# Performance work log

Hardware: AMD Instinct MI355X
Metric: run time of the kernel (lower is better)

The kernel has to match this reference:

```python
import jax, jax.numpy as jnp
import numpy as np

DIM = 768
NUM_HEADS = 12
HEAD_DIM = DIM // NUM_HEADS
ALL_HEAD_DIM = HEAD_DIM * NUM_HEADS
SCALE = HEAD_DIM ** -0.5


def setup_inputs() -> dict:
    key = jax.random.key(0)
    k1, k2, k3, k4 = jax.random.split(key, 4)
    B, N = 8, 1024
    x = jax.random.normal(k1, (B, N, DIM), dtype=jnp.float32)
    # qkv_bias=False -> no qkv bias; proj has bias (nn.Linear default)
    w_qkv = jax.random.normal(k2, (DIM, 3 * ALL_HEAD_DIM), dtype=jnp.float32) * (DIM ** -0.5)
    w_proj = jax.random.normal(k3, (ALL_HEAD_DIM, DIM), dtype=jnp.float32) * (ALL_HEAD_DIM ** -0.5)
    b_proj = jax.random.normal(k4, (DIM,), dtype=jnp.float32) * 0.02
    return {"x": x, "w_qkv": w_qkv, "w_proj": w_proj, "b_proj": b_proj}


def reference(x, w_qkv, w_proj, b_proj):
    B, N, C = x.shape
    qkv = (x @ w_qkv).reshape(B, N, 3, NUM_HEADS, HEAD_DIM)
    qkv = jnp.transpose(qkv, (2, 0, 3, 1, 4))  # [3, B, H, N, D]
    q, k, v = qkv[0], qkv[1], qkv[2]
    attn = jax.nn.softmax(jnp.einsum('bhnd,bhmd->bhnm', q * SCALE, k), axis=-1)
    out = jnp.einsum('bhnm,bhmd->bhnd', attn, v)  # [B, H, N, D]
    out = jnp.transpose(out, (0, 2, 1, 3)).reshape(B, N, ALL_HEAD_DIM)
    return out @ w_proj + b_proj
```

## Files before the change

kernel.cpp:

```cpp
#include <hip/hip_runtime.h>
#include <hip/hip_bf16.h>

#define NH 12
#define HD 64
#define SEQ 1024
#define BATCH 8
#define DIM 768
#define QKVN 2304
#define ROWS 8192

typedef __bf16 bf16x8 __attribute__((ext_vector_type(8)));
typedef float f32x4 __attribute__((ext_vector_type(4)));
typedef unsigned short u16x8 __attribute__((ext_vector_type(8)));
typedef unsigned short u16x4 __attribute__((ext_vector_type(4)));
typedef short s16x4 __attribute__((ext_vector_type(4)));

__device__ __forceinline__ unsigned short f2bf(float f) {
  union { float f; unsigned int u; } c; c.f = f;
  unsigned int u = c.u;
  u += 0x7fffu + ((u >> 16) & 1u);
  return (unsigned short)(u >> 16);
}

__device__ __forceinline__ unsigned int pk_bf16(float a, float b) {
  union { __hip_bfloat162 h; unsigned int w; } u;
  u.h = __float22bfloat162_rn(float2{a, b});
  return u.w;
}

__device__ __forceinline__ float exp2_fast(float x) {
  float r;
  asm("v_exp_f32 %0, %1" : "=v"(r) : "v"(x));
  return r;
}

__device__ __forceinline__ void gload_lds16(const unsigned short* g, unsigned short* l) {
  __builtin_amdgcn_global_load_lds(
      (const __attribute__((address_space(1))) void*)g,
      (__attribute__((address_space(3))) void*)l, 16, 0, 0);
}

__device__ __forceinline__ void tr_tile(const float* __restrict__ src, unsigned short* __restrict__ dst,
                                        int R, int C, int bx, int by, float tile[32][33]) {
  int tx = threadIdx.x & 31, ty = threadIdx.x >> 5;
  int c0 = bx * 32, r0 = by * 32;
#pragma unroll
  for (int i = 0; i < 4; ++i)
    tile[ty + i * 8][tx] = src[(size_t)(r0 + ty + i * 8) * C + c0 + tx];
  __syncthreads();
#pragma unroll
  for (int i = 0; i < 4; ++i)
    dst[(size_t)(c0 + ty + i * 8) * R + r0 + tx] = f2bf(tile[tx][ty + i * 8]);
}

__global__ void prep_kernel(const float* __restrict__ x, unsigned short* __restrict__ xb,
                            const float* __restrict__ w_qkv, unsigned short* __restrict__ wqkvT,
                            const float* __restrict__ w_proj, unsigned short* __restrict__ wprojT) {
  __shared__ float tile[32][33];
  int blk = blockIdx.x;
  if (blk < 6144) {
    int i = blk * 256 + threadIdx.x;
    float4 v = ((const float4*)x)[i];
    unsigned int lo = pk_bf16(v.x, v.y), hi = pk_bf16(v.z, v.w);
    union { unsigned int w[2]; u16x4 o; } u; u.w[0] = lo; u.w[1] = hi;
    ((u16x4*)xb)[i] = u.o;
  } else if (blk < 6144 + 1728) {
    int t = blk - 6144;
    tr_tile(w_qkv, wqkvT, DIM, QKVN, t % 72, t / 72, tile);
  } else {
    int t = blk - 6144 - 1728;
    tr_tile(w_proj, wprojT, DIM, DIM, t % 24, t / 24, tile);
  }
}

template <bool BF16_OUT, bool SCALE_Q>
__global__ __launch_bounds__(256, 3) void gemm192(
    const unsigned short* __restrict__ A, const unsigned short* __restrict__ BT,
    void* __restrict__ Cout, const float* __restrict__ bias,
    int M, int N, int K, int nbyXCD) {
  __shared__ unsigned short As[2][128 * 32];
  __shared__ unsigned short Bs[2][192 * 32];
  const int tid = threadIdx.x;
  const int wave = tid >> 6, lane = tid & 63, quad = lane >> 4, l16 = lane & 15;
  const int wm = wave >> 1, wn = wave & 1;
  const int g = blockIdx.x & 7, bi = blockIdx.x >> 3;
  const int by = g * nbyXCD + (bi % nbyXCD);
  const int bx = bi / nbyXCD;
  const int bm = by * 128, bn = bx * 192;

  const int r0 = tid >> 2, kc0 = (tid & 3) * 8;
  const unsigned short* Ag = A + (size_t)(bm + r0) * K + kc0;
  const unsigned short* Bg = BT + (size_t)(bn + r0) * K + kc0;
  unsigned short* AsB = &As[0][0];
  unsigned short* BsB = &Bs[0][0];
  const int wdst = (tid & ~63) * 8;

#define STAGE_G(kt, b) do {                                                   \
    int koff_ = (kt) * 32;                                                    \
    gload_lds16(Ag + koff_,                    AsB + (b) * 4096 + wdst);      \
    gload_lds16(Ag + koff_ + (size_t)64 * K,   AsB + (b) * 4096 + wdst + 2048);\
    gload_lds16(Bg + koff_,                    BsB + (b) * 6144 + wdst);      \
    gload_lds16(Bg + koff_ + (size_t)64 * K,   BsB + (b) * 6144 + wdst + 2048);\
    gload_lds16(Bg + koff_ + (size_t)128 * K,  BsB + (b) * 6144 + wdst + 4096);\
  } while (0)

  f32x4 zero4 = {0.f, 0.f, 0.f, 0.f};
  f32x4 acc[4][6];
#pragma unroll
  for (int i = 0; i < 4; ++i)
#pragma unroll
    for (int j = 0; j < 6; ++j) acc[i][j] = zero4;

  const int nkt = K >> 5;
  STAGE_G(0, 0);
  for (int kt = 0; kt < nkt; ++kt) {
    __syncthreads();
    if (kt + 1 < nkt) STAGE_G(kt + 1, (kt + 1) & 1);
    const unsigned short* Ab = AsB + (kt & 1) * 4096;
    const unsigned short* Bb = BsB + (kt & 1) * 6144;
    bf16x8 af[4], bf[6];
#pragma unroll
    for (int mt = 0; mt < 4; ++mt)
      af[mt] = *(const bf16x8*)&Ab[(wm * 64 + mt * 16 + l16) * 32 + quad * 8];
#pragma unroll
    for (int nt = 0; nt < 6; ++nt)
      bf[nt] = *(const bf16x8*)&Bb[(wn * 96 + nt * 16 + l16) * 32 + quad * 8];
#pragma unroll
    for (int mt = 0; mt < 4; ++mt)
#pragma unroll
      for (int nt = 0; nt < 6; ++nt)
        acc[mt][nt] = __builtin_amdgcn_mfma_f32_16x16x32_bf16(af[mt], bf[nt], acc[mt][nt], 0, 0, 0);
  }
#undef STAGE_G

#pragma unroll
  for (int mt = 0; mt < 4; ++mt)
#pragma unroll
    for (int nt = 0; nt < 6; ++nt) {
      int col = bn + wn * 96 + nt * 16 + l16;
      float bv = BF16_OUT ? 0.f : bias[col];
      float scl = (SCALE_Q && col < DIM) ? 0.18033688011112042f : 1.0f;
#pragma unroll
      for (int r = 0; r < 4; ++r) {
        int row = bm + wm * 64 + mt * 16 + quad * 4 + r;
        float v = acc[mt][nt][r];
        if (BF16_OUT)
          ((unsigned short*)Cout)[(size_t)row * N + col] = f2bf(v * scl);
        else
          ((float*)Cout)[(size_t)row * N + col] = v + bv;
      }
    }
}

__global__ __launch_bounds__(256, 4) void gemm64_proj(
    const unsigned short* __restrict__ A, const unsigned short* __restrict__ BT,
    float* __restrict__ Cout, const float* __restrict__ bias,
    int M, int N, int K, int nbyXCD) {
  __shared__ unsigned short As[2][128 * 64];
  __shared__ unsigned short Bs[2][64 * 64];
  const int tid = threadIdx.x;
  const int wave = tid >> 6, lane = tid & 63, quad = lane >> 4, l16 = lane & 15;
  const int g = blockIdx.x & 7, bi = blockIdx.x >> 3;
  const int by = g * nbyXCD + (bi % nbyXCD);
  const int bx = bi / nbyXCD;
  const int bm = by * 128, bn = bx * 64;

  const int r0 = tid >> 3;
  const int csw = ((tid & 7) ^ (r0 & 7)) * 8;
  const unsigned short* Ag = A + (size_t)(bm + r0) * K + csw;
  const unsigned short* Bg = BT + (size_t)(bn + r0) * K + csw;
  unsigned short* AsB = &As[0][0];
  unsigned short* BsB = &Bs[0][0];
  const int wdst = (tid & ~63) * 8;

#define STAGE_P(kt, b) do {                                                     \
    int koff_ = (kt) * 64;                                                      \
    gload_lds16(Ag + koff_,                   AsB + (b) * 8192 + wdst);         \
    gload_lds16(Ag + koff_ + (size_t)32 * K,  AsB + (b) * 8192 + wdst + 2048);  \
    gload_lds16(Ag + koff_ + (size_t)64 * K,  AsB + (b) * 8192 + wdst + 4096);  \
    gload_lds16(Ag + koff_ + (size_t)96 * K,  AsB + (b) * 8192 + wdst + 6144);  \
    gload_lds16(Bg + koff_,                   BsB + (b) * 4096 + wdst);         \
    gload_lds16(Bg + koff_ + (size_t)32 * K,  BsB + (b) * 4096 + wdst + 2048);  \
  } while (0)

  f32x4 zero4 = {0.f, 0.f, 0.f, 0.f};
  f32x4 acc[2][4];
#pragma unroll
  for (int i = 0; i < 2; ++i)
#pragma unroll
    for (int j = 0; j < 4; ++j) acc[i][j] = zero4;

  const int nkt = K >> 6;
  STAGE_P(0, 0);
  for (int kt = 0; kt < nkt; ++kt) {
    __syncthreads();
    if (kt + 1 < nkt) STAGE_P(kt + 1, (kt + 1) & 1);
    const unsigned short* Ab = AsB + (kt & 1) * 8192;
    const unsigned short* Bb = BsB + (kt & 1) * 4096;
#pragma unroll
    for (int kk = 0; kk < 2; ++kk) {
      const int pc = ((kk * 4 + quad) ^ (l16 & 7)) * 8;
      bf16x8 af[2], bf[4];
#pragma unroll
      for (int mt = 0; mt < 2; ++mt)
        af[mt] = *(const bf16x8*)&Ab[(wave * 32 + mt * 16 + l16) * 64 + pc];
#pragma unroll
      for (int nt = 0; nt < 4; ++nt)
        bf[nt] = *(const bf16x8*)&Bb[(nt * 16 + l16) * 64 + pc];
#pragma unroll
      for (int mt = 0; mt < 2; ++mt)
#pragma unroll
        for (int nt = 0; nt < 4; ++nt)
          acc[mt][nt] = __builtin_amdgcn_mfma_f32_16x16x32_bf16(af[mt], bf[nt], acc[mt][nt], 0, 0, 0);
    }
  }
#undef STAGE_P

#pragma unroll
  for (int mt = 0; mt < 2; ++mt)
#pragma unroll
    for (int nt = 0; nt < 4; ++nt) {
      int col = bn + nt * 16 + l16;
      float bv = bias[col];
#pragma unroll
      for (int r = 0; r < 4; ++r) {
        int row = bm + wave * 32 + mt * 16 + quad * 4 + r;
        Cout[(size_t)row * N + col] = acc[mt][nt][r] + bv;
      }
    }
}

#define VS 76
__global__ __launch_bounds__(512, 6) void attn_kernel(
    const unsigned short* __restrict__ qkv, unsigned short* __restrict__ out) {
  __shared__ unsigned short Ks[2][64 * 64];
  __shared__ unsigned short Vts[2][64 * VS];

  const int tid = threadIdx.x;
  const int wave = tid >> 6, lane = tid & 63, quad = lane >> 4, l16 = lane & 15;
  const int x = blockIdx.x;
  const int qt = (x >> 3) & 7;
  const int bh = (x & 7) + 8 * (x >> 6);
  const int b = bh / NH, h = bh % NH;
  const int qcol = h * HD, kcol = DIM + h * HD, vcol = 2 * DIM + h * HD;
  const int rowQ0 = b * SEQ + qt * 128;
  const int rowKV0 = b * SEQ;

  const int kk_s = tid >> 8, rem_s = tid & 255, n_s = rem_s >> 2, kc_s = rem_s & 3;
  const unsigned short* kgp = qkv + (size_t)(rowKV0 + n_s) * QKVN + kcol + kk_s * 32 + kc_s * 8;
  unsigned short* klp = &Ks[0][0] + (tid & ~63) * 8;
  const int vn = tid & 63, vd0 = (tid >> 6) * 8;
  const unsigned short* vgp = qkv + (size_t)(rowKV0 + vn) * QKVN + vcol + vd0;

  bf16x8 qf[2];
  {
    const unsigned short* qp = qkv + (size_t)(rowQ0 + wave * 16 + l16) * QKVN + qcol + quad * 8;
    qf[0] = *(const bf16x8*)qp;
    qf[1] = *(const bf16x8*)(qp + 32);
  }

  gload_lds16(kgp, klp);
  {
    u16x8 v0 = *(const u16x8*)vgp;
    unsigned short* vb = &Vts[0][0];
#pragma unroll
    for (int e = 0; e < 8; ++e)
      vb[(vd0 + e) * VS + vn] = v0[e];
  }

  f32x4 zero4 = {0.f, 0.f, 0.f, 0.f};
  f32x4 o[4];
#pragma unroll
  for (int dt = 0; dt < 4; ++dt) o[dt] = zero4;
  float lsum = 0.f;

  for (int jt = 0; jt < 16; ++jt) {
    __syncthreads();
    u16x8 vnext;
    if (jt < 15) {
      gload_lds16(kgp + (size_t)(jt + 1) * 64 * QKVN, klp + ((jt + 1) & 1) * 4096);
      vnext = *(const u16x8*)(vgp + (size_t)(jt + 1) * 64 * QKVN);
    }

    const unsigned short* Kb = &Ks[jt & 1][0];
    const unsigned short* Vb = &Vts[jt & 1][0];

    f32x4 s[4];
#pragma unroll
    for (int nt = 0; nt < 4; ++nt) s[nt] = zero4;
    __builtin_amdgcn_s_setprio(1);
#pragma unroll
    for (int kk = 0; kk < 2; ++kk)
#pragma unroll
      for (int nt = 0; nt < 4; ++nt) {
        bf16x8 kf = *(const bf16x8*)&Kb[kk * 2048 + (nt * 16 + l16) * 32 + quad * 8];
        s[nt] = __builtin_amdgcn_mfma_f32_16x16x32_bf16(kf, qf[kk], s[nt], 0, 0, 0);
      }
    __builtin_amdgcn_s_setprio(0);

    s16x4 pf[4];
#pragma unroll
    for (int nt = 0; nt < 4; ++nt) {
      float p0 = exp2_fast(s[nt][0]);
      float p1 = exp2_fast(s[nt][1]);
      float p2 = exp2_fast(s[nt][2]);
      float p3 = exp2_fast(s[nt][3]);
      lsum += (p0 + p1) + (p2 + p3);
      union { unsigned int w[2]; s16x4 v; } u;
      u.w[0] = pk_bf16(p0, p1);
      u.w[1] = pk_bf16(p2, p3);
      pf[nt] = u.v;
    }

    __builtin_amdgcn_s_setprio(1);
#pragma unroll
    for (int nt = 0; nt < 4; ++nt)
#pragma unroll
      for (int dt = 0; dt < 4; ++dt) {
        s16x4 vv = *(const s16x4*)&Vb[(dt * 16 + l16) * VS + nt * 16 + quad * 4];
        o[dt] = __builtin_amdgcn_mfma_f32_16x16x16bf16_1k(pf[nt], vv, o[dt], 0, 0, 0);
      }
    __builtin_amdgcn_s_setprio(0);

    if (jt < 15) {
      unsigned short* vb = &Vts[(jt + 1) & 1][0];
#pragma unroll
      for (int e = 0; e < 8; ++e)
        vb[(vd0 + e) * VS + vn] = vnext[e];
    }
  }

  float l = lsum;
  l += __shfl_xor(l, 16);
  l += __shfl_xor(l, 32);
#pragma unroll
  for (int r = 0; r < 4; ++r) {
    float inv = 1.f / __shfl(l, quad * 4 + r);
    int row = rowQ0 + wave * 16 + quad * 4 + r;
#pragma unroll
    for (int dt = 0; dt < 4; ++dt)
      out[(size_t)row * DIM + h * HD + dt * 16 + l16] = f2bf(o[dt][r] * inv);
  }
}

extern "C" void kernel_launch(void* const* d_in, const int* in_sizes, int n_in,
                              void* d_out, int out_size, void* d_ws, size_t ws_size,
                              hipStream_t stream) {
  const float* x = (const float*)d_in[0];
  const float* w_qkv = (const float*)d_in[1];
  const float* w_proj = (const float*)d_in[2];
  const float* b_proj = (const float*)d_in[3];
  float* outp = (float*)d_out;

  unsigned short* xb = (unsigned short*)d_ws;
  unsigned short* wqkvT = xb + (size_t)ROWS * DIM;
  unsigned short* wprojT = wqkvT + (size_t)QKVN * DIM;
  unsigned short* qkvb = wprojT + (size_t)DIM * DIM;
  unsigned short* attnb = xb;

  prep_kernel<<<dim3(6144 + 1728 + 576), 256, 0, stream>>>(x, xb, w_qkv, wqkvT, w_proj, wprojT);
  gemm192<true, true><<<dim3(768), 256, 0, stream>>>(xb, wqkvT, qkvb, nullptr, ROWS, QKVN, DIM, 8);
  attn_kernel<<<dim3(8 * 96), 512, 0, stream>>>(qkvb, attnb);
  gemm64_proj<<<dim3(768), 256, 0, stream>>>(attnb, wprojT, outp, b_proj, ROWS, DIM, DIM, 8);
}
```

Before: 177.7 us.

## Split attention keys across wave pairs so each K/V fragment feeds two query subtiles

Waves are paired. Each pair owns 32 query rows, and each wave in the pair handles half of every 64-key tile. Every K fragment and V fragment read from LDS now feeds two MFMAs, one per 16-row query subtile, which roughly halves LDS read traffic per unit of MFMA work. The two half-results, the partial O accumulators and row sums, are combined at the end through an LDS scratch area that reuses the K/V buffers. The cost is an extra sync and reduction step and twice as many accumulator registers per wave.

```diff
diff --git a/kernel.cpp b/kernel.cpp
--- a/kernel.cpp
+++ b/kernel.cpp
@@ -233,11 +233,13 @@
 #define VS 76
 __global__ __launch_bounds__(512, 6) void attn_kernel(
     const unsigned short* __restrict__ qkv, unsigned short* __restrict__ out) {
-  __shared__ unsigned short Ks[2][64 * 64];
-  __shared__ unsigned short Vts[2][64 * VS];
+  __shared__ unsigned short lds[2 * 64 * 64 + 2 * 64 * VS];
+  unsigned short* Ks = lds;
+  unsigned short* Vts = lds + 2 * 64 * 64;
 
   const int tid = threadIdx.x;
   const int wave = tid >> 6, lane = tid & 63, quad = lane >> 4, l16 = lane & 15;
+  const int qg = wave >> 1, kh = wave & 1;
   const int x = blockIdx.x;
   const int qt = (x >> 3) & 7;
   const int bh = (x & 7) + 8 * (x >> 6);
@@ -248,31 +250,34 @@
 
   const int kk_s = tid >> 8, rem_s = tid & 255, n_s = rem_s >> 2, kc_s = rem_s & 3;
   const unsigned short* kgp = qkv + (size_t)(rowKV0 + n_s) * QKVN + kcol + kk_s * 32 + kc_s * 8;
-  unsigned short* klp = &Ks[0][0] + (tid & ~63) * 8;
+  unsigned short* klp = Ks + (tid & ~63) * 8;
   const int vn = tid & 63, vd0 = (tid >> 6) * 8;
   const unsigned short* vgp = qkv + (size_t)(rowKV0 + vn) * QKVN + vcol + vd0;
 
-  bf16x8 qf[2];
-  {
-    const unsigned short* qp = qkv + (size_t)(rowQ0 + wave * 16 + l16) * QKVN + qcol + quad * 8;
-    qf[0] = *(const bf16x8*)qp;
-    qf[1] = *(const bf16x8*)(qp + 32);
+  bf16x8 qf[2][2];
+#pragma unroll
+  for (int sub = 0; sub < 2; ++sub) {
+    const unsigned short* qp = qkv + (size_t)(rowQ0 + qg * 32 + sub * 16 + l16) * QKVN + qcol + quad * 8;
+    qf[sub][0] = *(const bf16x8*)qp;
+    qf[sub][1] = *(const bf16x8*)(qp + 32);
   }
 
   gload_lds16(kgp, klp);
   {
     u16x8 v0 = *(const u16x8*)vgp;
-    unsigned short* vb = &Vts[0][0];
+    unsigned short* vb = Vts;
 #pragma unroll
     for (int e = 0; e < 8; ++e)
       vb[(vd0 + e) * VS + vn] = v0[e];
   }
 
   f32x4 zero4 = {0.f, 0.f, 0.f, 0.f};
-  f32x4 o[4];
-#pragma unroll
-  for (int dt = 0; dt < 4; ++dt) o[dt] = zero4;
-  float lsum = 0.f;
+  f32x4 o[2][4];
+#pragma unroll
+  for (int sub = 0; sub < 2; ++sub)
+#pragma unroll
+    for (int dt = 0; dt < 4; ++dt) o[sub][dt] = zero4;
+  float lsum[2] = {0.f, 0.f};
 
   for (int jt = 0; jt < 16; ++jt) {
     __syncthreads();
@@ -282,64 +287,98 @@
       vnext = *(const u16x8*)(vgp + (size_t)(jt + 1) * 64 * QKVN);
     }
 
-    const unsigned short* Kb = &Ks[jt & 1][0];
-    const unsigned short* Vb = &Vts[jt & 1][0];
-
-    f32x4 s[4];
-#pragma unroll
-    for (int nt = 0; nt < 4; ++nt) s[nt] = zero4;
+    const unsigned short* Kb = Ks + (jt & 1) * 4096;
+    const unsigned short* Vb = Vts + (jt & 1) * (64 * VS);
+
+    f32x4 s[2][2];
+#pragma unroll
+    for (int sub = 0; sub < 2; ++sub)
+#pragma unroll
+      for (int nt = 0; nt < 2; ++nt) s[sub][nt] = zero4;
     __builtin_amdgcn_s_setprio(1);
 #pragma unroll
     for (int kk = 0; kk < 2; ++kk)
 #pragma unroll
-      for (int nt = 0; nt < 4; ++nt) {
-        bf16x8 kf = *(const bf16x8*)&Kb[kk * 2048 + (nt * 16 + l16) * 32 + quad * 8];
-        s[nt] = __builtin_amdgcn_mfma_f32_16x16x32_bf16(kf, qf[kk], s[nt], 0, 0, 0);
+      for (int nt = 0; nt < 2; ++nt) {
+        bf16x8 kf = *(const bf16x8*)&Kb[kk * 2048 + (kh * 32 + nt * 16 + l16) * 32 + quad * 8];
+        s[0][nt] = __builtin_amdgcn_mfma_f32_16x16x32_bf16(kf, qf[0][kk], s[0][nt], 0, 0, 0);
+        s[1][nt] = __builtin_amdgcn_mfma_f32_16x16x32_bf16(kf, qf[1][kk], s[1][nt], 0, 0, 0);
       }
     __builtin_amdgcn_s_setprio(0);
 
-    s16x4 pf[4];
-#pragma unroll
-    for (int nt = 0; nt < 4; ++nt) {
-      float p0 = exp2_fast(s[nt][0]);
-      float p1 = exp2_fast(s[nt][1]);
-      float p2 = exp2_fast(s[nt][2]);
-      float p3 = exp2_fast(s[nt][3]);
-      lsum += (p0 + p1) + (p2 + p3);
-      union { unsigned int w[2]; s16x4 v; } u;
-      u.w[0] = pk_bf16(p0, p1);
-      u.w[1] = pk_bf16(p2, p3);
-      pf[nt] = u.v;
-    }
+    s16x4 pf[2][2];
+#pragma unroll
+    for (int sub = 0; sub < 2; ++sub)
+#pragma unroll
+      for (int nt = 0; nt < 2; ++nt) {
+        float p0 = exp2_fast(s[sub][nt][0]);
+        float p1 = exp2_fast(s[sub][nt][1]);
+        float p2 = exp2_fast(s[sub][nt][2]);
+        float p3 = exp2_fast(s[sub][nt][3]);
+        lsum[sub] += (p0 + p1) + (p2 + p3);
+        union { unsigned int w[2]; s16x4 v; } u;
+        u.w[0] = pk_bf16(p0, p1);
+        u.w[1] = pk_bf16(p2, p3);
+        pf[sub][nt] = u.v;
+      }
 
     __builtin_amdgcn_s_setprio(1);
 #pragma unroll
-    for (int nt = 0; nt < 4; ++nt)
+    for (int nt = 0; nt < 2; ++nt)
 #pragma unroll
       for (int dt = 0; dt < 4; ++dt) {
-        s16x4 vv = *(const s16x4*)&Vb[(dt * 16 + l16) * VS + nt * 16 + quad * 4];
-        o[dt] = __builtin_amdgcn_mfma_f32_16x16x16bf16_1k(pf[nt], vv, o[dt], 0, 0, 0);
+        s16x4 vv = *(const s16x4*)&Vb[(dt * 16 + l16) * VS + kh * 32 + nt * 16 + quad * 4];
+        o[0][dt] = __builtin_amdgcn_mfma_f32_16x16x16bf16_1k(pf[0][nt], vv, o[0][dt], 0, 0, 0);
+        o[1][dt] = __builtin_amdgcn_mfma_f32_16x16x16bf16_1k(pf[1][nt], vv, o[1][dt], 0, 0, 0);
       }
     __builtin_amdgcn_s_setprio(0);
 
     if (jt < 15) {
-      unsigned short* vb = &Vts[(jt + 1) & 1][0];
+      unsigned short* vb = Vts + ((jt + 1) & 1) * (64 * VS);
 #pragma unroll
       for (int e = 0; e < 8; ++e)
         vb[(vd0 + e) * VS + vn] = vnext[e];
     }
   }
 
-  float l = lsum;
-  l += __shfl_xor(l, 16);
-  l += __shfl_xor(l, 32);
-#pragma unroll
-  for (int r = 0; r < 4; ++r) {
-    float inv = 1.f / __shfl(l, quad * 4 + r);
-    int row = rowQ0 + wave * 16 + quad * 4 + r;
-#pragma unroll
-    for (int dt = 0; dt < 4; ++dt)
-      out[(size_t)row * DIM + h * HD + dt * 16 + l16] = f2bf(o[dt][r] * inv);
+  __syncthreads();
+  float* sc = (float*)lds;
+  float* scl = sc + 4 * 64 * 32;
+  if (kh) {
+    float* dst = sc + (qg * 64 + lane) * 32;
+#pragma unroll
+    for (int sub = 0; sub < 2; ++sub)
+#pragma unroll
+      for (int dt = 0; dt < 4; ++dt)
+        *(f32x4*)(dst + sub * 16 + dt * 4) = o[sub][dt];
+    scl[(qg * 64 + lane) * 2 + 0] = lsum[0];
+    scl[(qg * 64 + lane) * 2 + 1] = lsum[1];
+  }
+  __syncthreads();
+  if (!kh) {
+    const float* src = sc + (qg * 64 + lane) * 32;
+#pragma unroll
+    for (int sub = 0; sub < 2; ++sub)
+#pragma unroll
+      for (int dt = 0; dt < 4; ++dt)
+        o[sub][dt] += *(const f32x4*)(src + sub * 16 + dt * 4);
+    lsum[0] += scl[(qg * 64 + lane) * 2 + 0];
+    lsum[1] += scl[(qg * 64 + lane) * 2 + 1];
+
+#pragma unroll
+    for (int sub = 0; sub < 2; ++sub) {
+      float l = lsum[sub];
+      l += __shfl_xor(l, 16);
+      l += __shfl_xor(l, 32);
+#pragma unroll
+      for (int r = 0; r < 4; ++r) {
+        float inv = 1.f / __shfl(l, quad * 4 + r);
+        int row = rowQ0 + qg * 32 + sub * 16 + quad * 4 + r;
+#pragma unroll
+        for (int dt = 0; dt < 4; ++dt)
+          out[(size_t)row * DIM + h * HD + dt * 16 + l16] = f2bf(o[sub][dt][r] * inv);
+      }
+    }
   }
 }
 
```

New measurement: 210.3 us. +18.3%, slower.
